# Kernel optimization log

Measured on AMD Instinct MI355X. Metric: run time of the kernel, lower is better.

The kernel has to match this reference:

```python
import jax, jax.numpy as jnp
import numpy as np
import math

PRE_D = 2048   # pre_d_model (scaled from 8192)
D = 4096       # d_model (scaled from 16384)
N = 64         # d_state (scaled from 128)
K = 4          # d_conv
EXP = 2
L = 128        # sequence_length
DI1 = EXP * PRE_D
DI2 = EXP * D
DTR1 = math.ceil(PRE_D / 16)
DTR2 = math.ceil(D / 16)


def _sinusoid(max_len, d):
    pe = np.zeros((max_len, d), np.float32)
    pos = np.arange(max_len, dtype=np.float32)[:, None]
    div = np.exp(np.arange(0, d, 2, dtype=np.float32) * (-math.log(10000.0) / d))
    pe[:, 0::2] = np.sin(pos * div)
    pe[:, 1::2] = np.cos(pos * div)
    return jnp.asarray(pe)


def _mamba_params(key, d_in, d_out, di, dtr, n, k):
    ks = jax.random.split(key, 6)
    s = 0.02
    dt = jnp.exp(jax.random.uniform(ks[4], (di,)) * (math.log(0.1) - math.log(1e-3)) + math.log(1e-3))
    return dict(
        in_proj=jax.random.normal(ks[0], (2 * di, d_in)) * s,
        conv_w=jax.random.normal(ks[1], (di, k)) * s,
        conv_b=jnp.zeros((di,)),
        x_proj=jax.random.normal(ks[2], (dtr + 2 * n, di)) * s,
        dt_w=jax.random.normal(ks[3], (di, dtr)) * s,
        dt_b=jnp.log(jnp.expm1(dt)),  # softplus^-1 of dt init
        A_log=jnp.log(jnp.tile(jnp.arange(1, n + 1, dtype=jnp.float32), (di, 1))),
        D=jnp.ones((di,)),
        out_proj=jax.random.normal(ks[5], (d_out, di)) * s,
    )


def setup_inputs() -> dict:
    key = jax.random.key(0)
    k1, k2, k3, k4 = jax.random.split(key, 4)
    inp = {
        'pe': _sinusoid(L, PRE_D),                              # (L, PRE_D)
        'to_cond_w': jax.random.normal(k3, (PRE_D, 1)) * 0.02,  # Linear(1 -> PRE_D)
        'to_cond_b': jnp.zeros((PRE_D,)),
        'condition': jax.random.normal(k4, (1,)),
        'batch': 1,
    }
    for pref, p in (('m1_', _mamba_params(k1, PRE_D, PRE_D, DI1, DTR1, N, K)),
                    ('m2_', _mamba_params(k2, PRE_D, D, DI2, DTR2, N, K))):
        for name, v in p.items():
            inp[pref + name] = v
    return inp


def _silu(x):
    return x * jax.nn.sigmoid(x)


def _mamba(x, in_w, cw, cb, xp_w, dt_w, dt_b, A_log, Dp, out_w, dtr, n):
    # x: (B, L, d_in)
    xz = x @ in_w.T                     # (B, L, 2*di)
    xr, z = jnp.split(xz, 2, axis=-1)
    kk = cw.shape[1]
    Lx = xr.shape[1]
    xpad = jnp.pad(xr, ((0, 0), (kk - 1, 0), (0, 0)))  # causal pad
    conv = sum(cw[:, i] * xpad[:, i:i + Lx, :] for i in range(kk)) + cb
    xr = _silu(conv)
    dbc = xr @ xp_w.T                   # (B, L, dtr + 2n)
    dt = dbc[..., :dtr]
    Bm = dbc[..., dtr:dtr + n]
    Cm = dbc[..., dtr + n:]
    dt = jax.nn.softplus(dt @ dt_w.T + dt_b)           # (B, L, di)
    A = -jnp.exp(A_log)                                 # (di, n)
    dA = jnp.exp(jnp.einsum('bld,dn->bldn', dt, A))
    dBx = jnp.einsum('bld,bln,bld->bldn', dt, Bm, xr)

    def comb(c1, c2):
        a1, b1 = c1
        a2, b2 = c2
        return a2 * a1, a2 * b1 + b2

    _, h = jax.lax.associative_scan(comb, (dA, dBx), axis=1)  # (B, L, di, n)
    y = jnp.einsum('bldn,bln->bld', h, Cm) + xr * Dp
    y = y * _silu(z)
    return y @ out_w.T


def reference(pe, to_cond_w, to_cond_b, condition,
              m1_in_proj, m1_conv_w, m1_conv_b, m1_x_proj, m1_dt_w, m1_dt_b, m1_A_log, m1_D, m1_out_proj,
              m2_in_proj, m2_conv_w, m2_conv_b, m2_x_proj, m2_dt_w, m2_dt_b, m2_A_log, m2_D, m2_out_proj,
              batch):
    cond = condition.reshape(-1, 1, 1)
    c = jnp.einsum('bli,oi->blo', cond, to_cond_w) + to_cond_b   # (Bc,1,PRE_D)
    x = jnp.tile(pe[None], (batch, 1, 1)) + c                    # (B, L, PRE_D)
    x = _mamba(x, m1_in_proj, m1_conv_w, m1_conv_b, m1_x_proj, m1_dt_w, m1_dt_b,
               m1_A_log, m1_D, m1_out_proj, DTR1, N)
    x = _mamba(x, m2_in_proj, m2_conv_w, m2_conv_b, m2_x_proj, m2_dt_w, m2_dt_b,
               m2_A_log, m2_D, m2_out_proj, DTR2, N)
    return x
```

## Files before the change

### kernel.cpp

```cpp
#include <hip/hip_runtime.h>
#include <hip/hip_bf16.h>
#include <math.h>


typedef __attribute__((ext_vector_type(8))) short short8_t;
typedef __attribute__((ext_vector_type(4))) float f32x4;

__device__ __forceinline__ float sigmoidf_(float x) {
  return 1.0f / (1.0f + __expf(-x));
}
__device__ __forceinline__ float softplusf_(float x) {
  return fmaxf(x, 0.0f) + log1pf(expf(-fabsf(x)));
}
__device__ __forceinline__ void splitbf(float f, ushort& h, ushort& lo) {
  __hip_bfloat16 hb = __float2bfloat16(f);
  h = *reinterpret_cast<ushort*>(&hb);
  float hf = __bfloat162float(hb);
  __hip_bfloat16 lb = __float2bfloat16(f - hf);
  lo = *reinterpret_cast<ushort*>(&lb);
}

__global__ __launch_bounds__(256) void k_prep(const float* __restrict__ pe,
                                              const float* __restrict__ cw,
                                              const float* __restrict__ cb,
                                              const float* __restrict__ cond,
                                              ushort* __restrict__ xh,
                                              ushort* __restrict__ xl) {
  int i = blockIdx.x * 256 + threadIdx.x;
  int d = i & 2047;
  float v = pe[i] + cond[0] * cw[d] + cb[d];
  splitbf(v, xh[i], xl[i]);
}

#define KSTEP 32
__global__ __launch_bounds__(256, 2) void k_gemm(const ushort* __restrict__ Xh,
                                                 const ushort* __restrict__ Xl,
                                                 int ldx,
                                                 const float* __restrict__ W, int ldw,
                                                 float* __restrict__ P,
                                                 int N, int Ks) {
  __shared__ ushort As[2][2][4][128][8];

  const int n0   = blockIdx.x * 128;
  const int s    = blockIdx.z;
  const int kbeg = s * Ks;
  const int t    = threadIdx.x;
  const int l    = t & 63;
  const int w    = t >> 6;
  const int wm   = w >> 1;
  const int wn   = w & 1;
  const int lr   = l & 15;
  const int lg   = l >> 4;

  f32x4 acc[4][4];
#pragma unroll
  for (int mi = 0; mi < 4; ++mi)
#pragma unroll
    for (int ni = 0; ni < 4; ++ni) acc[mi][ni] = (f32x4)(0.0f);

  const int srow = t >> 1;
  const int skq  = (t & 1) * 2;
  const ushort* pXh = Xh + (size_t)srow * ldx + kbeg + skq * 8;
  const ushort* pXl = Xl + (size_t)srow * ldx + kbeg + skq * 8;
  const int arow = 64 * wm + lr;
  const float* pW = W + (size_t)(n0 + 64 * wn + lr) * ldw + kbeg + 8 * lg;
  const size_t wstep = (size_t)16 * ldw;

  {
    *(short8_t*)&As[0][0][skq][srow][0]     = *(const short8_t*)(pXh);
    *(short8_t*)&As[0][0][skq + 1][srow][0] = *(const short8_t*)(pXh + 8);
    *(short8_t*)&As[0][1][skq][srow][0]     = *(const short8_t*)(pXl);
    *(short8_t*)&As[0][1][skq + 1][srow][0] = *(const short8_t*)(pXl + 8);
  }
  float wcur[32];
#pragma unroll
  for (int ni = 0; ni < 4; ++ni) {
    *(float4*)&wcur[ni * 8]     = *(const float4*)(pW + ni * wstep);
    *(float4*)&wcur[ni * 8 + 4] = *(const float4*)(pW + ni * wstep + 4);
  }
  __syncthreads();

  const int nIter = Ks / KSTEP;
  for (int j = 0; j < nIter; ++j) {
    const int bi = j & 1;
    const bool more = (j + 1 < nIter);
    const int ko = (j + 1) * KSTEP;

    float wnxt[32];
    short8_t anh0, anh1, anl0, anl1;
    if (more) {
#pragma unroll
      for (int ni = 0; ni < 4; ++ni) {
        *(float4*)&wnxt[ni * 8]     = *(const float4*)(pW + ko + ni * wstep);
        *(float4*)&wnxt[ni * 8 + 4] = *(const float4*)(pW + ko + ni * wstep + 4);
      }
      anh0 = *(const short8_t*)(pXh + ko);
      anh1 = *(const short8_t*)(pXh + ko + 8);
      anl0 = *(const short8_t*)(pXl + ko);
      anl1 = *(const short8_t*)(pXl + ko + 8);
    }

    short8_t bh[4], bl[4];
#pragma unroll
    for (int ni = 0; ni < 4; ++ni)
#pragma unroll
      for (int e = 0; e < 8; ++e) {
        const float f = wcur[ni * 8 + e];
        __hip_bfloat16 hb = __float2bfloat16(f);
        const float hf = __bfloat162float(hb);
        __hip_bfloat16 lb = __float2bfloat16(f - hf);
        bh[ni][e] = (short)*reinterpret_cast<ushort*>(&hb);
        bl[ni][e] = (short)*reinterpret_cast<ushort*>(&lb);
      }

#pragma unroll
    for (int mi = 0; mi < 4; ++mi) {
      const short8_t ah = *(const short8_t*)&As[bi][0][lg][arow + 16 * mi][0];
      const short8_t al = *(const short8_t*)&As[bi][1][lg][arow + 16 * mi][0];
#pragma unroll
      for (int ni = 0; ni < 4; ++ni) {
        acc[mi][ni] = __builtin_amdgcn_mfma_f32_16x16x32_bf16(ah, bh[ni], acc[mi][ni], 0, 0, 0);
        acc[mi][ni] = __builtin_amdgcn_mfma_f32_16x16x32_bf16(ah, bl[ni], acc[mi][ni], 0, 0, 0);
        acc[mi][ni] = __builtin_amdgcn_mfma_f32_16x16x32_bf16(al, bh[ni], acc[mi][ni], 0, 0, 0);
      }
    }

    if (more) {
      *(short8_t*)&As[bi ^ 1][0][skq][srow][0]     = anh0;
      *(short8_t*)&As[bi ^ 1][0][skq + 1][srow][0] = anh1;
      *(short8_t*)&As[bi ^ 1][1][skq][srow][0]     = anl0;
      *(short8_t*)&As[bi ^ 1][1][skq + 1][srow][0] = anl1;
#pragma unroll
      for (int e2 = 0; e2 < 32; ++e2) wcur[e2] = wnxt[e2];
    }
    __syncthreads();
  }

  float* Pd = P + (size_t)s * 128 * N + n0 + 64 * wn;
#pragma unroll
  for (int mi = 0; mi < 4; ++mi)
#pragma unroll
    for (int ni = 0; ni < 4; ++ni) {
#pragma unroll
      for (int j = 0; j < 4; ++j) {
        const int m = 64 * wm + 16 * mi + 4 * lg + j;
        Pd[(size_t)m * N + 16 * ni + lr] = acc[mi][ni][j];
      }
    }
}

__global__ __launch_bounds__(256) void k_reduce(const float* __restrict__ P,
                                                float* __restrict__ Y,
                                                ushort* __restrict__ Yh,
                                                ushort* __restrict__ Yl,
                                                int MN, int N, int S, int ep,
                                                const float* __restrict__ bias) {
  int i = (blockIdx.x * 256 + threadIdx.x) * 4;
  if (i >= MN) return;
  float4 v = *(const float4*)&P[i];
  for (int s = 1; s < S; ++s) {
    float4 p = *(const float4*)&P[(size_t)s * MN + i];
    v.x += p.x; v.y += p.y; v.z += p.z; v.w += p.w;
  }
  if (ep & 1) {
    int n = i % N;
    const float4 b = *(const float4*)&bias[n];
    v.x = softplusf_(v.x + b.x);
    v.y = softplusf_(v.y + b.y);
    v.z = softplusf_(v.z + b.z);
    v.w = softplusf_(v.w + b.w);
  }
  if (ep & 4) *(float4*)&Y[i] = v;
  if (ep & 2) {
    ushort4 h4, l4;
    splitbf(v.x, h4.x, l4.x);
    splitbf(v.y, h4.y, l4.y);
    splitbf(v.z, h4.z, l4.z);
    splitbf(v.w, h4.w, l4.w);
    *(ushort4*)&Yh[i] = h4;
    *(ushort4*)&Yl[i] = l4;
  }
}

__global__ __launch_bounds__(256) void k_reduceA(const float* __restrict__ P,
                                                 float* __restrict__ Y, int MN) {
  int g = blockIdx.y;
  int i = (blockIdx.x * 256 + threadIdx.x) * 4;
  if (i >= MN) return;
  const float* Pp = P + (size_t)g * 8 * MN;
  float4 v = *(const float4*)&Pp[i];
  for (int s = 1; s < 8; ++s) {
    float4 p = *(const float4*)&Pp[(size_t)s * MN + i];
    v.x += p.x; v.y += p.y; v.z += p.z; v.w += p.w;
  }
  *(float4*)&Y[(size_t)g * MN + i] = v;
}

__global__ __launch_bounds__(256) void k_conv_silu(const float* __restrict__ xz,
                                                   const float* __restrict__ cw,
                                                   const float* __restrict__ cb,
                                                   float* __restrict__ xc,
                                                   ushort* __restrict__ xch,
                                                   ushort* __restrict__ xcl,
                                                   int DI, int lg2DI) {
  int i = blockIdx.x * 256 + threadIdx.x;
  int l = i >> lg2DI;
  int d = i & (DI - 1);
  const float4 w = *(const float4*)&cw[d * 4];
  const float* xr = xz + d;
  int ld = 2 * DI;
  float s = cb[d];
  s += w.w * xr[l * ld];
  if (l >= 1) s += w.z * xr[(l - 1) * ld];
  if (l >= 2) s += w.y * xr[(l - 2) * ld];
  if (l >= 3) s += w.x * xr[(l - 3) * ld];
  float v = s * sigmoidf_(s);
  xc[i] = v;
  splitbf(v, xch[i], xcl[i]);
}

__global__ __launch_bounds__(256) void k_scan(const float* __restrict__ dt,
                                              const float* __restrict__ xc,
                                              const float* __restrict__ dbc,
                                              const float* __restrict__ A_log,
                                              const float* __restrict__ Dp,
                                              float* __restrict__ y,
                                              int DI, int DTR) {
  __shared__ float cs[4][32][65];
  const int wid = threadIdx.x >> 6;
  const int n   = threadIdx.x & 63;
  const int d   = blockIdx.x * 4 + wid;
  const int du  = __builtin_amdgcn_readfirstlane(d);
  const float A  = -__expf(A_log[(size_t)du * 64 + n]);
  const float Dd = Dp[du];
  const int ldbc = DTR + 128;
  const float* Bp = dbc + DTR + n;
  const float* Cp = dbc + DTR + 64 + n;
  float h = 0.0f;
  for (int l0 = 0; l0 < 128; l0 += 32) {
#pragma unroll 8
    for (int l = l0; l < l0 + 32; ++l) {
      float dtv = dt[(size_t)l * DI + du];
      float xcv = xc[(size_t)l * DI + du];
      float dA  = __expf(dtv * A);
      float bx  = dtv * xcv;
      h = fmaf(dA, h, bx * Bp[(size_t)l * ldbc]);
      cs[wid][l - l0][n] = h * Cp[(size_t)l * ldbc];
    }
    __syncthreads();
    const int r = n & 31, hf = n >> 5;
    float ssum = 0.0f;
#pragma unroll
    for (int j = 0; j < 32; ++j) ssum += cs[wid][r][hf * 32 + j];
    ssum += __shfl_xor(ssum, 32, 64);
    if (n < 32) {
      int ll = l0 + r;
      float xcv = xc[(size_t)ll * DI + du];
      y[(size_t)ll * DI + du] = ssum + xcv * Dd;
    }
    __syncthreads();
  }
}

__global__ __launch_bounds__(256) void k_gate(const float* __restrict__ yb,
                                              const float* __restrict__ xz,
                                              ushort* __restrict__ yh,
                                              ushort* __restrict__ yl,
                                              int DI, int lg2DI) {
  int i = blockIdx.x * 256 + threadIdx.x;
  int l = i >> lg2DI;
  int d = i & (DI - 1);
  float z = xz[((size_t)l << (lg2DI + 1)) + DI + d];
  float v = yb[i] * (z * sigmoidf_(z));
  splitbf(v, yh[i], yl[i]);
}

struct GemmCtx {
  float* part;
  float* part2;
  long long cap;
};

static inline void gemm(const ushort* Xh, const ushort* Xl, int ldx,
                        const float* W, int ldw,
                        float* dstF, ushort* dstH, ushort* dstL,
                        int N, int K, int Sdes, int ep,
                        const float* bias, const GemmCtx& cx, hipStream_t stream) {
  int S = Sdes;
  if (S > K / KSTEP) S = K / KSTEP;
  if (S < 1) S = 1;
  while (S > 1 && (long long)S * 128 * N > cx.cap) S >>= 1;
  const int Ks = K / S;
  const bool direct = (S == 1 && ep == 4);
  dim3 g(N / 128, 1, S);
  float* dst = direct ? dstF : cx.part;
  k_gemm<<<g, 256, 0, stream>>>(Xh, Xl, ldx, W, ldw, dst, N, Ks);
  if (direct) return;
  const int MN = 128 * N;
  const int rb = (MN / 4 + 255) / 256;
  if (S <= 16) {
    k_reduce<<<rb, 256, 0, stream>>>(cx.part, dstF, dstH, dstL, MN, N, S, ep, bias);
  } else {
    k_reduceA<<<dim3(rb, S / 8), 256, 0, stream>>>(cx.part, cx.part2, MN);
    k_reduce<<<rb, 256, 0, stream>>>(cx.part2, dstF, dstH, dstL, MN, N, S / 8, ep, bias);
  }
}

extern "C" void kernel_launch(void* const* d_in, const int* in_sizes, int n_in,
                              void* d_out, int out_size, void* d_ws, size_t ws_size,
                              hipStream_t stream) {
  const float* pe        = (const float*)d_in[0];
  const float* to_cond_w = (const float*)d_in[1];
  const float* to_cond_b = (const float*)d_in[2];
  const float* condition = (const float*)d_in[3];
  const int o = (in_sizes[4] == 1) ? 5 : 4;
  const float* m1_in_proj  = (const float*)d_in[o + 0];
  const float* m1_conv_w   = (const float*)d_in[o + 1];
  const float* m1_conv_b   = (const float*)d_in[o + 2];
  const float* m1_x_proj   = (const float*)d_in[o + 3];
  const float* m1_dt_w     = (const float*)d_in[o + 4];
  const float* m1_dt_b     = (const float*)d_in[o + 5];
  const float* m1_A_log    = (const float*)d_in[o + 6];
  const float* m1_D        = (const float*)d_in[o + 7];
  const float* m1_out_proj = (const float*)d_in[o + 8];
  const float* m2_in_proj  = (const float*)d_in[o + 9];
  const float* m2_conv_w   = (const float*)d_in[o + 10];
  const float* m2_conv_b   = (const float*)d_in[o + 11];
  const float* m2_x_proj   = (const float*)d_in[o + 12];
  const float* m2_dt_w     = (const float*)d_in[o + 13];
  const float* m2_dt_b     = (const float*)d_in[o + 14];
  const float* m2_A_log    = (const float*)d_in[o + 15];
  const float* m2_D        = (const float*)d_in[o + 16];
  const float* m2_out_proj = (const float*)d_in[o + 17];

  float* ws = (float*)d_ws;
  float*  xz   = ws;
  float*  xc   = ws + 2097152;
  float*  dbc  = ws + 3145728;
  float*  dtb  = ws + 3194880;
  float*  yb   = ws + 4243456;
  ushort* x0h  = (ushort*)(ws + 5292032);
  ushort* x0l  = (ushort*)(ws + 5423104);
  ushort* xch  = (ushort*)(ws + 5554176);
  ushort* xcl  = (ushort*)(ws + 6078464);
  ushort* dbch = (ushort*)(ws + 6602752);
  ushort* dbcl = (ushort*)(ws + 6627328);
  ushort* ybh  = (ushort*)(ws + 6651904);
  ushort* ybl  = (ushort*)(ws + 7176192);
  ushort* midh = (ushort*)(ws + 7700480);
  ushort* midl = (ushort*)(ws + 7831552);
  float*  part2 = ws + 7962624;
  float*  part  = ws + 8486912;

  GemmCtx cx;
  cx.part = part;
  cx.part2 = part2;
  cx.cap = (long long)(ws_size / 4) - 8486912;
  if (cx.cap < 0) cx.cap = 0;

  k_prep<<<1024, 256, 0, stream>>>(pe, to_cond_w, to_cond_b, condition, x0h, x0l);

  gemm(x0h, x0l, 2048, m1_in_proj, 2048, xz, nullptr, nullptr,
       8192, 2048, 8, 4, nullptr, cx, stream);
  k_conv_silu<<<(128 * 4096) / 256, 256, 0, stream>>>(xz, m1_conv_w, m1_conv_b,
                                                      xc, xch, xcl, 4096, 12);
  gemm(xch, xcl, 4096, m1_x_proj, 4096, dbc, dbch, dbcl,
       256, 4096, 64, 6, nullptr, cx, stream);
  gemm(dbch, dbcl, 256, m1_dt_w, 128, dtb, nullptr, nullptr,
       4096, 128, 4, 5, m1_dt_b, cx, stream);
  k_scan<<<1024, 256, 0, stream>>>(dtb, xc, dbc, m1_A_log, m1_D, yb, 4096, 128);
  k_gate<<<(128 * 4096) / 256, 256, 0, stream>>>(yb, xz, ybh, ybl, 4096, 12);
  gemm(ybh, ybl, 4096, m1_out_proj, 4096, nullptr, midh, midl,
       2048, 4096, 16, 2, nullptr, cx, stream);

  gemm(midh, midl, 2048, m2_in_proj, 2048, xz, nullptr, nullptr,
       16384, 2048, 4, 4, nullptr, cx, stream);
  k_conv_silu<<<(128 * 8192) / 256, 256, 0, stream>>>(xz, m2_conv_w, m2_conv_b,
                                                      xc, xch, xcl, 8192, 13);
  gemm(xch, xcl, 8192, m2_x_proj, 8192, dbc, dbch, dbcl,
       384, 8192, 64, 6, nullptr, cx, stream);
  gemm(dbch, dbcl, 384, m2_dt_w, 256, dtb, nullptr, nullptr,
       8192, 256, 4, 5, m2_dt_b, cx, stream);
  k_scan<<<2048, 256, 0, stream>>>(dtb, xc, dbc, m2_A_log, m2_D, yb, 8192, 256);
  k_gate<<<(128 * 8192) / 256, 256, 0, stream>>>(yb, xz, ybh, ybl, 8192, 13);
  gemm(ybh, ybl, 8192, m2_out_proj, 8192, (float*)d_out, nullptr, nullptr,
       4096, 8192, 8, 4, nullptr, cx, stream);
}
```

Measured before the change: 401.8 us.

## Load GEMM A fragments directly from global memory and raise split-K counts

The GEMM kernel no longer stages the bf16 hi/lo activation tile through LDS with barriers. Each wave now loads its A fragments straight from global memory (served from L2/L1 across waves) and double-buffers the weight registers with a two-way unrolled loop. This removes the LDS writes and __syncthreads and frees shared memory, but it adds redundant global A loads across the wn waves and raises register pressure. Split-K counts are also increased for three GEMMs to put more blocks in flight, at the cost of more partial-sum traffic in the reduce.

```diff
diff --git a/kernel.cpp b/kernel.cpp
--- a/kernel.cpp
+++ b/kernel.cpp
@@ -39,8 +39,6 @@
                                                  const float* __restrict__ W, int ldw,
                                                  float* __restrict__ P,
                                                  int N, int Ks) {
-  __shared__ ushort As[2][2][4][128][8];
-
   const int n0   = blockIdx.x * 128;
   const int s    = blockIdx.z;
   const int kbeg = s * Ks;
@@ -58,83 +56,73 @@
 #pragma unroll
     for (int ni = 0; ni < 4; ++ni) acc[mi][ni] = (f32x4)(0.0f);
 
-  const int srow = t >> 1;
-  const int skq  = (t & 1) * 2;
-  const ushort* pXh = Xh + (size_t)srow * ldx + kbeg + skq * 8;
-  const ushort* pXl = Xl + (size_t)srow * ldx + kbeg + skq * 8;
-  const int arow = 64 * wm + lr;
+  const ushort* pAh = Xh + (size_t)(64 * wm + lr) * ldx + kbeg + 8 * lg;
+  const ushort* pAl = Xl + (size_t)(64 * wm + lr) * ldx + kbeg + 8 * lg;
   const float* pW = W + (size_t)(n0 + 64 * wn + lr) * ldw + kbeg + 8 * lg;
+  const size_t astep = (size_t)16 * ldx;
   const size_t wstep = (size_t)16 * ldw;
 
-  {
-    *(short8_t*)&As[0][0][skq][srow][0]     = *(const short8_t*)(pXh);
-    *(short8_t*)&As[0][0][skq + 1][srow][0] = *(const short8_t*)(pXh + 8);
-    *(short8_t*)&As[0][1][skq][srow][0]     = *(const short8_t*)(pXl);
-    *(short8_t*)&As[0][1][skq + 1][srow][0] = *(const short8_t*)(pXl + 8);
-  }
-  float wcur[32];
-#pragma unroll
-  for (int ni = 0; ni < 4; ++ni) {
-    *(float4*)&wcur[ni * 8]     = *(const float4*)(pW + ni * wstep);
-    *(float4*)&wcur[ni * 8 + 4] = *(const float4*)(pW + ni * wstep + 4);
-  }
-  __syncthreads();
+  float wv0[32], wv1[32];
+  short8_t ah[4], al[4];
+
+#define LOADW0(KO)                                                            \
+  do {                                                                        \
+    _Pragma("unroll") for (int ni = 0; ni < 4; ++ni) {                        \
+      *(float4*)&wv0[ni * 8]     = *(const float4*)(pW + ni * wstep + (KO));  \
+      *(float4*)&wv0[ni * 8 + 4] = *(const float4*)(pW + ni * wstep + (KO) + 4); \
+    }                                                                         \
+  } while (0)
+#define LOADW1(KO)                                                            \
+  do {                                                                        \
+    _Pragma("unroll") for (int ni = 0; ni < 4; ++ni) {                        \
+      *(float4*)&wv1[ni * 8]     = *(const float4*)(pW + ni * wstep + (KO));  \
+      *(float4*)&wv1[ni * 8 + 4] = *(const float4*)(pW + ni * wstep + (KO) + 4); \
+    }                                                                         \
+  } while (0)
+#define LOADA(KO)                                                             \
+  do {                                                                        \
+    _Pragma("unroll") for (int mi = 0; mi < 4; ++mi) {                        \
+      ah[mi] = *(const short8_t*)(pAh + mi * astep + (KO));                   \
+      al[mi] = *(const short8_t*)(pAl + mi * astep + (KO));                   \
+    }                                                                         \
+  } while (0)
+#define COMPUTE(WV)                                                           \
+  do {                                                                        \
+    _Pragma("unroll") for (int ni = 0; ni < 4; ++ni) {                        \
+      short8_t bh, bl;                                                        \
+      _Pragma("unroll") for (int e = 0; e < 8; ++e) {                         \
+        const float f = WV[ni * 8 + e];                                       \
+        __hip_bfloat16 hb = __float2bfloat16(f);                              \
+        const float hf = __bfloat162float(hb);                                \
+        __hip_bfloat16 lb = __float2bfloat16(f - hf);                         \
+        bh[e] = (short)*reinterpret_cast<ushort*>(&hb);                       \
+        bl[e] = (short)*reinterpret_cast<ushort*>(&lb);                       \
+      }                                                                       \
+      _Pragma("unroll") for (int mi = 0; mi < 4; ++mi) {                      \
+        acc[mi][ni] = __builtin_amdgcn_mfma_f32_16x16x32_bf16(ah[mi], bh, acc[mi][ni], 0, 0, 0); \
+        acc[mi][ni] = __builtin_amdgcn_mfma_f32_16x16x32_bf16(al[mi], bh, acc[mi][ni], 0, 0, 0); \
+        acc[mi][ni] = __builtin_amdgcn_mfma_f32_16x16x32_bf16(ah[mi], bl, acc[mi][ni], 0, 0, 0); \
+      }                                                                       \
+    }                                                                         \
+  } while (0)
 
   const int nIter = Ks / KSTEP;
-  for (int j = 0; j < nIter; ++j) {
-    const int bi = j & 1;
-    const bool more = (j + 1 < nIter);
-    const int ko = (j + 1) * KSTEP;
-
-    float wnxt[32];
-    short8_t anh0, anh1, anl0, anl1;
-    if (more) {
-#pragma unroll
-      for (int ni = 0; ni < 4; ++ni) {
-        *(float4*)&wnxt[ni * 8]     = *(const float4*)(pW + ko + ni * wstep);
-        *(float4*)&wnxt[ni * 8 + 4] = *(const float4*)(pW + ko + ni * wstep + 4);
-      }
-      anh0 = *(const short8_t*)(pXh + ko);
-      anh1 = *(const short8_t*)(pXh + ko + 8);
-      anl0 = *(const short8_t*)(pXl + ko);
-      anl1 = *(const short8_t*)(pXl + ko + 8);
-    }
-
-    short8_t bh[4], bl[4];
-#pragma unroll
-    for (int ni = 0; ni < 4; ++ni)
-#pragma unroll
-      for (int e = 0; e < 8; ++e) {
-        const float f = wcur[ni * 8 + e];
-        __hip_bfloat16 hb = __float2bfloat16(f);
-        const float hf = __bfloat162float(hb);
-        __hip_bfloat16 lb = __float2bfloat16(f - hf);
-        bh[ni][e] = (short)*reinterpret_cast<ushort*>(&hb);
-        bl[ni][e] = (short)*reinterpret_cast<ushort*>(&lb);
-      }
-
-#pragma unroll
-    for (int mi = 0; mi < 4; ++mi) {
-      const short8_t ah = *(const short8_t*)&As[bi][0][lg][arow + 16 * mi][0];
-      const short8_t al = *(const short8_t*)&As[bi][1][lg][arow + 16 * mi][0];
-#pragma unroll
-      for (int ni = 0; ni < 4; ++ni) {
-        acc[mi][ni] = __builtin_amdgcn_mfma_f32_16x16x32_bf16(ah, bh[ni], acc[mi][ni], 0, 0, 0);
-        acc[mi][ni] = __builtin_amdgcn_mfma_f32_16x16x32_bf16(ah, bl[ni], acc[mi][ni], 0, 0, 0);
-        acc[mi][ni] = __builtin_amdgcn_mfma_f32_16x16x32_bf16(al, bh[ni], acc[mi][ni], 0, 0, 0);
-      }
-    }
-
-    if (more) {
-      *(short8_t*)&As[bi ^ 1][0][skq][srow][0]     = anh0;
-      *(short8_t*)&As[bi ^ 1][0][skq + 1][srow][0] = anh1;
-      *(short8_t*)&As[bi ^ 1][1][skq][srow][0]     = anl0;
-      *(short8_t*)&As[bi ^ 1][1][skq + 1][srow][0] = anl1;
-#pragma unroll
-      for (int e2 = 0; e2 < 32; ++e2) wcur[e2] = wnxt[e2];
-    }
-    __syncthreads();
-  }
+  LOADW0(0);
+  int j = 0;
+  for (;;) {
+    LOADA(j * KSTEP);
+    if (j + 1 < nIter) LOADW1((j + 1) * KSTEP);
+    COMPUTE(wv0);
+    ++j; if (j == nIter) break;
+    LOADA(j * KSTEP);
+    if (j + 1 < nIter) LOADW0((j + 1) * KSTEP);
+    COMPUTE(wv1);
+    ++j; if (j == nIter) break;
+  }
+#undef LOADW0
+#undef LOADW1
+#undef LOADA
+#undef COMPUTE
 
   float* Pd = P + (size_t)s * 128 * N + n0 + 64 * wn;
 #pragma unroll
@@ -142,9 +130,9 @@
 #pragma unroll
     for (int ni = 0; ni < 4; ++ni) {
 #pragma unroll
-      for (int j = 0; j < 4; ++j) {
-        const int m = 64 * wm + 16 * mi + 4 * lg + j;
-        Pd[(size_t)m * N + 16 * ni + lr] = acc[mi][ni][j];
+      for (int jj = 0; jj < 4; ++jj) {
+        const int m = 64 * wm + 16 * mi + 4 * lg + jj;
+        Pd[(size_t)m * N + 16 * ni + lr] = acc[mi][ni][jj];
       }
     }
 }
@@ -371,7 +359,7 @@
   k_scan<<<1024, 256, 0, stream>>>(dtb, xc, dbc, m1_A_log, m1_D, yb, 4096, 128);
   k_gate<<<(128 * 4096) / 256, 256, 0, stream>>>(yb, xz, ybh, ybl, 4096, 12);
   gemm(ybh, ybl, 4096, m1_out_proj, 4096, nullptr, midh, midl,
-       2048, 4096, 16, 2, nullptr, cx, stream);
+       2048, 4096, 32, 2, nullptr, cx, stream);
 
   gemm(midh, midl, 2048, m2_in_proj, 2048, xz, nullptr, nullptr,
        16384, 2048, 4, 4, nullptr, cx, stream);
@@ -380,9 +368,9 @@
   gemm(xch, xcl, 8192, m2_x_proj, 8192, dbc, dbch, dbcl,
        384, 8192, 64, 6, nullptr, cx, stream);
   gemm(dbch, dbcl, 384, m2_dt_w, 256, dtb, nullptr, nullptr,
-       8192, 256, 4, 5, m2_dt_b, cx, stream);
+       8192, 256, 8, 5, m2_dt_b, cx, stream);
   k_scan<<<2048, 256, 0, stream>>>(dtb, xc, dbc, m2_A_log, m2_D, yb, 8192, 256);
   k_gate<<<(128 * 8192) / 256, 256, 0, stream>>>(yb, xz, ybh, ybl, 8192, 13);
   gemm(ybh, ybl, 8192, m2_out_proj, 8192, (float*)d_out, nullptr, nullptr,
-       4096, 8192, 8, 4, nullptr, cx, stream);
-}
+       4096, 8192, 16, 4, nullptr, cx, stream);
+}
```

Result: slower. 414.3 us (+3.1%).

## Pre-pack activations into MFMA fragment layout and stage split weights through LDS

Applied to the files above, without the earlier changes.

Activations are now written by the producer kernels into a packed hi/lo bf16 layout that matches the MFMA fragment order, so the GEMM loads A fragments straight from global memory with no LDS staging. Weights are loaded with coalesced float4 rows, split once per element into hi/lo bf16, and shared through LDS. Before, each wave split its own weight fragments in registers, so every weight was split twice per block. Split-K factors are also retuned for several GEMMs. The trade-off is more global A traffic per wave, since four waves reload the same A fragments, and a larger workspace offset for the partial buffers.

```diff
diff --git a/kernel.cpp b/kernel.cpp
--- a/kernel.cpp
+++ b/kernel.cpp
@@ -19,27 +19,33 @@
   __hip_bfloat16 lb = __float2bfloat16(f - hf);
   lo = *reinterpret_cast<ushort*>(&lb);
 }
+__device__ __forceinline__ size_t poff(int l, int d) {
+  return (size_t)(d >> 5) * 8192 + (size_t)((d >> 3) & 3) * 1024 +
+         (size_t)l * 8 + (d & 7);
+}
 
 __global__ __launch_bounds__(256) void k_prep(const float* __restrict__ pe,
                                               const float* __restrict__ cw,
                                               const float* __restrict__ cb,
                                               const float* __restrict__ cond,
-                                              ushort* __restrict__ xh,
-                                              ushort* __restrict__ xl) {
+                                              ushort* __restrict__ xp) {
   int i = blockIdx.x * 256 + threadIdx.x;
   int d = i & 2047;
+  int l = i >> 11;
   float v = pe[i] + cond[0] * cw[d] + cb[d];
-  splitbf(v, xh[i], xl[i]);
+  ushort h, lo;
+  splitbf(v, h, lo);
+  size_t o = poff(l, d);
+  xp[o] = h;
+  xp[o + 4096] = lo;
 }
 
 #define KSTEP 32
-__global__ __launch_bounds__(256, 2) void k_gemm(const ushort* __restrict__ Xh,
-                                                 const ushort* __restrict__ Xl,
-                                                 int ldx,
+__global__ __launch_bounds__(256, 2) void k_gemm(const ushort* __restrict__ Ap,
                                                  const float* __restrict__ W, int ldw,
                                                  float* __restrict__ P,
                                                  int N, int Ks) {
-  __shared__ ushort As[2][2][4][128][8];
+  __shared__ ushort Ws[2][2][4][128][8];
 
   const int n0   = blockIdx.x * 128;
   const int s    = blockIdx.z;
@@ -58,80 +64,73 @@
 #pragma unroll
     for (int ni = 0; ni < 4; ++ni) acc[mi][ni] = (f32x4)(0.0f);
 
-  const int srow = t >> 1;
-  const int skq  = (t & 1) * 2;
-  const ushort* pXh = Xh + (size_t)srow * ldx + kbeg + skq * 8;
-  const ushort* pXl = Xl + (size_t)srow * ldx + kbeg + skq * 8;
+  const int srow = t >> 3;
+  const int sk16 = t & 7;
+  const int skb  = sk16 >> 1;
+  const int se0  = (sk16 & 1) * 4;
+  const float* pWg = W + (size_t)(n0 + srow) * ldw + kbeg + sk16 * 4;
+
+  const ushort* pAc = Ap + (size_t)(kbeg >> 5) * 8192;
   const int arow = 64 * wm + lr;
-  const float* pW = W + (size_t)(n0 + 64 * wn + lr) * ldw + kbeg + 8 * lg;
-  const size_t wstep = (size_t)16 * ldw;
-
-  {
-    *(short8_t*)&As[0][0][skq][srow][0]     = *(const short8_t*)(pXh);
-    *(short8_t*)&As[0][0][skq + 1][srow][0] = *(const short8_t*)(pXh + 8);
-    *(short8_t*)&As[0][1][skq][srow][0]     = *(const short8_t*)(pXl);
-    *(short8_t*)&As[0][1][skq + 1][srow][0] = *(const short8_t*)(pXl + 8);
-  }
-  float wcur[32];
-#pragma unroll
-  for (int ni = 0; ni < 4; ++ni) {
-    *(float4*)&wcur[ni * 8]     = *(const float4*)(pW + ni * wstep);
-    *(float4*)&wcur[ni * 8 + 4] = *(const float4*)(pW + ni * wstep + 4);
+  const int brow = 64 * wn + lr;
+
+  const int nIter = Ks / KSTEP;
+  float4 wv[4];
+
+#pragma unroll
+  for (int r = 0; r < 4; ++r)
+    wv[r] = *(const float4*)(pWg + (size_t)(r * 32) * ldw);
+#pragma unroll
+  for (int r = 0; r < 4; ++r) {
+    ushort4 h4, l4;
+    splitbf(wv[r].x, h4.x, l4.x); splitbf(wv[r].y, h4.y, l4.y);
+    splitbf(wv[r].z, h4.z, l4.z); splitbf(wv[r].w, h4.w, l4.w);
+    *(ushort4*)&Ws[0][0][skb][srow + 32 * r][se0] = h4;
+    *(ushort4*)&Ws[0][1][skb][srow + 32 * r][se0] = l4;
   }
   __syncthreads();
 
-  const int nIter = Ks / KSTEP;
   for (int j = 0; j < nIter; ++j) {
     const int bi = j & 1;
     const bool more = (j + 1 < nIter);
-    const int ko = (j + 1) * KSTEP;
-
-    float wnxt[32];
-    short8_t anh0, anh1, anl0, anl1;
+
+    const ushort* pAj = pAc + (size_t)j * 8192;
+    short8_t ah[4], al[4];
+#pragma unroll
+    for (int mi = 0; mi < 4; ++mi) {
+      const size_t fo = (size_t)lg * 1024 + (size_t)(arow + 16 * mi) * 8;
+      ah[mi] = *(const short8_t*)(pAj + fo);
+      al[mi] = *(const short8_t*)(pAj + 4096 + fo);
+    }
     if (more) {
+      const size_t ko = (size_t)(j + 1) * KSTEP;
+#pragma unroll
+      for (int r = 0; r < 4; ++r)
+        wv[r] = *(const float4*)(pWg + ko + (size_t)(r * 32) * ldw);
+    }
+    short8_t bh[4], bl[4];
+#pragma unroll
+    for (int ni = 0; ni < 4; ++ni) {
+      bh[ni] = *(const short8_t*)&Ws[bi][0][lg][brow + 16 * ni][0];
+      bl[ni] = *(const short8_t*)&Ws[bi][1][lg][brow + 16 * ni][0];
+    }
+#pragma unroll
+    for (int mi = 0; mi < 4; ++mi)
 #pragma unroll
       for (int ni = 0; ni < 4; ++ni) {
-        *(float4*)&wnxt[ni * 8]     = *(const float4*)(pW + ko + ni * wstep);
-        *(float4*)&wnxt[ni * 8 + 4] = *(const float4*)(pW + ko + ni * wstep + 4);
+        acc[mi][ni] = __builtin_amdgcn_mfma_f32_16x16x32_bf16(ah[mi], bh[ni], acc[mi][ni], 0, 0, 0);
+        acc[mi][ni] = __builtin_amdgcn_mfma_f32_16x16x32_bf16(al[mi], bh[ni], acc[mi][ni], 0, 0, 0);
+        acc[mi][ni] = __builtin_amdgcn_mfma_f32_16x16x32_bf16(ah[mi], bl[ni], acc[mi][ni], 0, 0, 0);
       }
-      anh0 = *(const short8_t*)(pXh + ko);
-      anh1 = *(const short8_t*)(pXh + ko + 8);
-      anl0 = *(const short8_t*)(pXl + ko);
-      anl1 = *(const short8_t*)(pXl + ko + 8);
-    }
-
-    short8_t bh[4], bl[4];
-#pragma unroll
-    for (int ni = 0; ni < 4; ++ni)
-#pragma unroll
-      for (int e = 0; e < 8; ++e) {
-        const float f = wcur[ni * 8 + e];
-        __hip_bfloat16 hb = __float2bfloat16(f);
-        const float hf = __bfloat162float(hb);
-        __hip_bfloat16 lb = __float2bfloat16(f - hf);
-        bh[ni][e] = (short)*reinterpret_cast<ushort*>(&hb);
-        bl[ni][e] = (short)*reinterpret_cast<ushort*>(&lb);
+    if (more) {
+#pragma unroll
+      for (int r = 0; r < 4; ++r) {
+        ushort4 h4, l4;
+        splitbf(wv[r].x, h4.x, l4.x); splitbf(wv[r].y, h4.y, l4.y);
+        splitbf(wv[r].z, h4.z, l4.z); splitbf(wv[r].w, h4.w, l4.w);
+        *(ushort4*)&Ws[bi ^ 1][0][skb][srow + 32 * r][se0] = h4;
+        *(ushort4*)&Ws[bi ^ 1][1][skb][srow + 32 * r][se0] = l4;
       }
-
-#pragma unroll
-    for (int mi = 0; mi < 4; ++mi) {
-      const short8_t ah = *(const short8_t*)&As[bi][0][lg][arow + 16 * mi][0];
-      const short8_t al = *(const short8_t*)&As[bi][1][lg][arow + 16 * mi][0];
-#pragma unroll
-      for (int ni = 0; ni < 4; ++ni) {
-        acc[mi][ni] = __builtin_amdgcn_mfma_f32_16x16x32_bf16(ah, bh[ni], acc[mi][ni], 0, 0, 0);
-        acc[mi][ni] = __builtin_amdgcn_mfma_f32_16x16x32_bf16(ah, bl[ni], acc[mi][ni], 0, 0, 0);
-        acc[mi][ni] = __builtin_amdgcn_mfma_f32_16x16x32_bf16(al, bh[ni], acc[mi][ni], 0, 0, 0);
-      }
-    }
-
-    if (more) {
-      *(short8_t*)&As[bi ^ 1][0][skq][srow][0]     = anh0;
-      *(short8_t*)&As[bi ^ 1][0][skq + 1][srow][0] = anh1;
-      *(short8_t*)&As[bi ^ 1][1][skq][srow][0]     = anl0;
-      *(short8_t*)&As[bi ^ 1][1][skq + 1][srow][0] = anl1;
-#pragma unroll
-      for (int e2 = 0; e2 < 32; ++e2) wcur[e2] = wnxt[e2];
     }
     __syncthreads();
   }
@@ -142,17 +141,16 @@
 #pragma unroll
     for (int ni = 0; ni < 4; ++ni) {
 #pragma unroll
-      for (int j = 0; j < 4; ++j) {
-        const int m = 64 * wm + 16 * mi + 4 * lg + j;
-        Pd[(size_t)m * N + 16 * ni + lr] = acc[mi][ni][j];
+      for (int jj = 0; jj < 4; ++jj) {
+        const int m = 64 * wm + 16 * mi + 4 * lg + jj;
+        Pd[(size_t)m * N + 16 * ni + lr] = acc[mi][ni][jj];
       }
     }
 }
 
 __global__ __launch_bounds__(256) void k_reduce(const float* __restrict__ P,
                                                 float* __restrict__ Y,
-                                                ushort* __restrict__ Yh,
-                                                ushort* __restrict__ Yl,
+                                                ushort* __restrict__ Yp,
                                                 int MN, int N, int S, int ep,
                                                 const float* __restrict__ bias) {
   int i = (blockIdx.x * 256 + threadIdx.x) * 4;
@@ -162,8 +160,9 @@
     float4 p = *(const float4*)&P[(size_t)s * MN + i];
     v.x += p.x; v.y += p.y; v.z += p.z; v.w += p.w;
   }
+  int n = i % N;
+  int l = i / N;
   if (ep & 1) {
-    int n = i % N;
     const float4 b = *(const float4*)&bias[n];
     v.x = softplusf_(v.x + b.x);
     v.y = softplusf_(v.y + b.y);
@@ -177,8 +176,9 @@
     splitbf(v.y, h4.y, l4.y);
     splitbf(v.z, h4.z, l4.z);
     splitbf(v.w, h4.w, l4.w);
-    *(ushort4*)&Yh[i] = h4;
-    *(ushort4*)&Yl[i] = l4;
+    size_t o = poff(l, n);
+    *(ushort4*)&Yp[o] = h4;
+    *(ushort4*)&Yp[o + 4096] = l4;
   }
 }
 
@@ -200,8 +200,7 @@
                                                    const float* __restrict__ cw,
                                                    const float* __restrict__ cb,
                                                    float* __restrict__ xc,
-                                                   ushort* __restrict__ xch,
-                                                   ushort* __restrict__ xcl,
+                                                   ushort* __restrict__ xcp,
                                                    int DI, int lg2DI) {
   int i = blockIdx.x * 256 + threadIdx.x;
   int l = i >> lg2DI;
@@ -216,7 +215,11 @@
   if (l >= 3) s += w.x * xr[(l - 3) * ld];
   float v = s * sigmoidf_(s);
   xc[i] = v;
-  splitbf(v, xch[i], xcl[i]);
+  ushort h, lo;
+  splitbf(v, h, lo);
+  size_t o = poff(l, d);
+  xcp[o] = h;
+  xcp[o + 4096] = lo;
 }
 
 __global__ __launch_bounds__(256) void k_scan(const float* __restrict__ dt,
@@ -264,15 +267,18 @@
 
 __global__ __launch_bounds__(256) void k_gate(const float* __restrict__ yb,
                                               const float* __restrict__ xz,
-                                              ushort* __restrict__ yh,
-                                              ushort* __restrict__ yl,
+                                              ushort* __restrict__ yp,
                                               int DI, int lg2DI) {
   int i = blockIdx.x * 256 + threadIdx.x;
   int l = i >> lg2DI;
   int d = i & (DI - 1);
   float z = xz[((size_t)l << (lg2DI + 1)) + DI + d];
   float v = yb[i] * (z * sigmoidf_(z));
-  splitbf(v, yh[i], yl[i]);
+  ushort h, lo;
+  splitbf(v, h, lo);
+  size_t o = poff(l, d);
+  yp[o] = h;
+  yp[o + 4096] = lo;
 }
 
 struct GemmCtx {
@@ -281,9 +287,8 @@
   long long cap;
 };
 
-static inline void gemm(const ushort* Xh, const ushort* Xl, int ldx,
-                        const float* W, int ldw,
-                        float* dstF, ushort* dstH, ushort* dstL,
+static inline void gemm(const ushort* Ap, const float* W, int ldw,
+                        float* dstF, ushort* dstP,
                         int N, int K, int Sdes, int ep,
                         const float* bias, const GemmCtx& cx, hipStream_t stream) {
   int S = Sdes;
@@ -294,15 +299,15 @@
   const bool direct = (S == 1 && ep == 4);
   dim3 g(N / 128, 1, S);
   float* dst = direct ? dstF : cx.part;
-  k_gemm<<<g, 256, 0, stream>>>(Xh, Xl, ldx, W, ldw, dst, N, Ks);
+  k_gemm<<<g, 256, 0, stream>>>(Ap, W, ldw, dst, N, Ks);
   if (direct) return;
   const int MN = 128 * N;
   const int rb = (MN / 4 + 255) / 256;
   if (S <= 16) {
-    k_reduce<<<rb, 256, 0, stream>>>(cx.part, dstF, dstH, dstL, MN, N, S, ep, bias);
+    k_reduce<<<rb, 256, 0, stream>>>(cx.part, dstF, dstP, MN, N, S, ep, bias);
   } else {
     k_reduceA<<<dim3(rb, S / 8), 256, 0, stream>>>(cx.part, cx.part2, MN);
-    k_reduce<<<rb, 256, 0, stream>>>(cx.part2, dstF, dstH, dstL, MN, N, S / 8, ep, bias);
+    k_reduce<<<rb, 256, 0, stream>>>(cx.part2, dstF, dstP, MN, N, S / 8, ep, bias);
   }
 }
 
@@ -339,50 +344,37 @@
   float*  dbc  = ws + 3145728;
   float*  dtb  = ws + 3194880;
   float*  yb   = ws + 4243456;
-  ushort* x0h  = (ushort*)(ws + 5292032);
-  ushort* x0l  = (ushort*)(ws + 5423104);
-  ushort* xch  = (ushort*)(ws + 5554176);
-  ushort* xcl  = (ushort*)(ws + 6078464);
-  ushort* dbch = (ushort*)(ws + 6602752);
-  ushort* dbcl = (ushort*)(ws + 6627328);
-  ushort* ybh  = (ushort*)(ws + 6651904);
-  ushort* ybl  = (ushort*)(ws + 7176192);
-  ushort* midh = (ushort*)(ws + 7700480);
-  ushort* midl = (ushort*)(ws + 7831552);
+  ushort* x0p  = (ushort*)(ws + 5292032);
+  ushort* xcp  = (ushort*)(ws + 5554176);
+  ushort* dbcp = (ushort*)(ws + 6602752);
+  ushort* ybp  = (ushort*)(ws + 6651904);
+  ushort* midp = (ushort*)(ws + 7700480);
   float*  part2 = ws + 7962624;
-  float*  part  = ws + 8486912;
+  float*  part  = ws + 8749056;
 
   GemmCtx cx;
   cx.part = part;
   cx.part2 = part2;
-  cx.cap = (long long)(ws_size / 4) - 8486912;
+  cx.cap = (long long)(ws_size / 4) - 8749056;
   if (cx.cap < 0) cx.cap = 0;
 
-  k_prep<<<1024, 256, 0, stream>>>(pe, to_cond_w, to_cond_b, condition, x0h, x0l);
-
-  gemm(x0h, x0l, 2048, m1_in_proj, 2048, xz, nullptr, nullptr,
-       8192, 2048, 8, 4, nullptr, cx, stream);
+  k_prep<<<1024, 256, 0, stream>>>(pe, to_cond_w, to_cond_b, condition, x0p);
+
+  gemm(x0p, m1_in_proj, 2048, xz, nullptr, 8192, 2048, 4, 4, nullptr, cx, stream);
   k_conv_silu<<<(128 * 4096) / 256, 256, 0, stream>>>(xz, m1_conv_w, m1_conv_b,
-                                                      xc, xch, xcl, 4096, 12);
-  gemm(xch, xcl, 4096, m1_x_proj, 4096, dbc, dbch, dbcl,
-       256, 4096, 64, 6, nullptr, cx, stream);
-  gemm(dbch, dbcl, 256, m1_dt_w, 128, dtb, nullptr, nullptr,
-       4096, 128, 4, 5, m1_dt_b, cx, stream);
+                                                      xc, xcp, 4096, 12);
+  gemm(xcp, m1_x_proj, 4096, dbc, dbcp, 256, 4096, 128, 6, nullptr, cx, stream);
+  gemm(dbcp, m1_dt_w, 128, dtb, nullptr, 4096, 128, 4, 5, m1_dt_b, cx, stream);
   k_scan<<<1024, 256, 0, stream>>>(dtb, xc, dbc, m1_A_log, m1_D, yb, 4096, 128);
-  k_gate<<<(128 * 4096) / 256, 256, 0, stream>>>(yb, xz, ybh, ybl, 4096, 12);
-  gemm(ybh, ybl, 4096, m1_out_proj, 4096, nullptr, midh, midl,
-       2048, 4096, 16, 2, nullptr, cx, stream);
-
-  gemm(midh, midl, 2048, m2_in_proj, 2048, xz, nullptr, nullptr,
-       16384, 2048, 4, 4, nullptr, cx, stream);
+  k_gate<<<(128 * 4096) / 256, 256, 0, stream>>>(yb, xz, ybp, 4096, 12);
+  gemm(ybp, m1_out_proj, 4096, nullptr, midp, 2048, 4096, 16, 2, nullptr, cx, stream);
+
+  gemm(midp, m2_in_proj, 2048, xz, nullptr, 16384, 2048, 2, 4, nullptr, cx, stream);
   k_conv_silu<<<(128 * 8192) / 256, 256, 0, stream>>>(xz, m2_conv_w, m2_conv_b,
-                                                      xc, xch, xcl, 8192, 13);
-  gemm(xch, xcl, 8192, m2_x_proj, 8192, dbc, dbch, dbcl,
-       384, 8192, 64, 6, nullptr, cx, stream);
-  gemm(dbch, dbcl, 384, m2_dt_w, 256, dtb, nullptr, nullptr,
-       8192, 256, 4, 5, m2_dt_b, cx, stream);
+                                                      xc, xcp, 8192, 13);
+  gemm(xcp, m2_x_proj, 8192, dbc, dbcp, 384, 8192, 128, 6, nullptr, cx, stream);
+  gemm(dbcp, m2_dt_w, 256, dtb, nullptr, 8192, 256, 4, 5, m2_dt_b, cx, stream);
   k_scan<<<2048, 256, 0, stream>>>(dtb, xc, dbc, m2_A_log, m2_D, yb, 8192, 256);
-  k_gate<<<(128 * 8192) / 256, 256, 0, stream>>>(yb, xz, ybh, ybl, 8192, 13);
-  gemm(ybh, ybl, 8192, m2_out_proj, 8192, (float*)d_out, nullptr, nullptr,
-       4096, 8192, 8, 4, nullptr, cx, stream);
-}
+  k_gate<<<(128 * 8192) / 256, 256, 0, stream>>>(yb, xz, ybp, 8192, 13);
+  gemm(ybp, m2_out_proj, 8192, (float*)d_out, nullptr, 4096, 8192, 8, 4, nullptr, cx, stream);
+}
```

Result: no change. 398.1 us (-0.9%).
